# Optimization experiments

Measured on AMD Instinct MI355X. Metric: run time of the kernel, lower is better.

The kernel has to match this reference:

```python
import jax, jax.numpy as jnp
import numpy as np

N = 4096
IN_F = 512
OUT_F = 64
N_HEADS = 8
ALPHA = 0.2
NEG_INF = -9e15


def setup_inputs() -> dict:
    key = jax.random.key(0)
    k1, k2, k3, k4 = jax.random.split(key, 4)
    h = jax.random.normal(k1, (N, IN_F), dtype=jnp.float32)
    adj = jax.random.randint(k2, (N, N), 0, 2, dtype=jnp.int32)
    W = jax.random.normal(k3, (IN_F, OUT_F * N_HEADS), dtype=jnp.float32) * (1.414 / np.sqrt(IN_F))
    a = jax.random.normal(k4, (2 * OUT_F, 1), dtype=jnp.float32) * 0.1
    return {"h": h, "adj": adj, "W": W, "a": a}


def reference(h, adj, W, a):
    # Wh: [N, H, F]
    Wh = (h @ W).reshape(N, N_HEADS, OUT_F)
    # The all-pairs concat + matmul with a ([2F,1], shared across heads)
    # decomposes exactly: e[i,j,h] = leakyrelu(Wh[i,h]@a[:F] + Wh[j,h]@a[F:])
    a_src = a[:OUT_F, 0]
    a_dst = a[OUT_F:, 0]
    src = jnp.einsum('nhf,f->nh', Wh, a_src)  # [N, H]
    dst = jnp.einsum('nhf,f->nh', Wh, a_dst)  # [N, H]
    e = src[:, None, :] + dst[None, :, :]      # [N, N, H]
    e = jnp.where(e > 0, e, ALPHA * e)         # leaky relu
    e = jnp.where(adj[:, :, None] > 0, e, NEG_INF)
    attention = jax.nn.softmax(e, axis=1)      # softmax over neighbors j
    h_prime = jnp.einsum('ijh,jhf->ihf', attention, Wh)  # [N, H, F]
    out = h_prime.reshape(N, N_HEADS * OUT_F)
    return jax.nn.elu(out)
```

## Files before the change

kernel.cpp:

```cpp
#include <hip/hip_runtime.h>
#include <hip/hip_bf16.h>


typedef unsigned short ushort_t;
typedef __attribute__((ext_vector_type(8))) short bf16x8;
typedef __attribute__((ext_vector_type(4))) float f32x4;

#define LOG2E 1.4426950408889634f

__device__ __forceinline__ ushort_t f2bf(float x) {
    unsigned u = __builtin_bit_cast(unsigned, x);
    u += 0x7FFFu + ((u >> 16) & 1u);
    return (ushort_t)(u >> 16);
}

__global__ __launch_bounds__(256) void transpose_w(const float* __restrict__ W,
                                                   ushort_t* __restrict__ WT) {
    __shared__ ushort_t t[32][33];
    int bx = blockIdx.x & 15, by = blockIdx.x >> 4;
    int tx = threadIdx.x & 31, ty = threadIdx.x >> 5;
#pragma unroll
    for (int i = 0; i < 32; i += 8)
        t[ty + i][tx] = f2bf(W[(by * 32 + ty + i) * 512 + bx * 32 + tx]);
    __syncthreads();
#pragma unroll
    for (int i = 0; i < 32; i += 8)
        WT[(bx * 32 + ty + i) * 512 + by * 32 + tx] = t[tx][ty + i];
}

__global__ __launch_bounds__(256, 4) void gemm_whT(const ushort_t* __restrict__ WT,
                                                   const float* __restrict__ h,
                                                   const float* __restrict__ a,
                                                   ushort_t* __restrict__ WhT,
                                                   float* __restrict__ expA,
                                                   float* __restrict__ expC,
                                                   float* __restrict__ expB,
                                                   float* __restrict__ expD) {
    __shared__ __align__(16) ushort_t Al[2][64][72];
    __shared__ __align__(16) ushort_t Bl[2][64][72];
    __shared__ float asrc[64], adst[64];
    __shared__ float sred[2][4][64];
    int tid = threadIdx.x;
    int wave = tid >> 6, lane = tid & 63, quad = lane >> 4, nn = lane & 15;
    int mb = blockIdx.x & 7, nb = blockIdx.x >> 3;
    if (tid < 64) {
        asrc[tid] = a[tid] * LOG2E;
        adst[tid] = a[64 + tid] * LOG2E;
    }
    int r = tid >> 2, s0 = tid & 3;
    const ushort_t* Ag = WT + (unsigned)((mb * 64 + r) * 512 + s0 * 8);
    const float* Bg = h + (unsigned)((nb * 64 + r) * 512 + s0 * 8);
    bf16x8 pA0 = *(const bf16x8*)(Ag);
    bf16x8 pA1 = *(const bf16x8*)(Ag + 32);
    float4 pb0 = *(const float4*)(Bg);
    float4 pb1 = *(const float4*)(Bg + 4);
    float4 pb2 = *(const float4*)(Bg + 32);
    float4 pb3 = *(const float4*)(Bg + 36);
    f32x4 acc[4] = {};
#pragma unroll 2
    for (int t = 0; t < 8; t++) {
        int cb = t & 1;
        *(bf16x8*)&Al[cb][r][s0 * 8] = pA0;
        *(bf16x8*)&Al[cb][r][s0 * 8 + 32] = pA1;
        bf16x8 bv;
        bv[0] = (short)f2bf(pb0.x); bv[1] = (short)f2bf(pb0.y);
        bv[2] = (short)f2bf(pb0.z); bv[3] = (short)f2bf(pb0.w);
        bv[4] = (short)f2bf(pb1.x); bv[5] = (short)f2bf(pb1.y);
        bv[6] = (short)f2bf(pb1.z); bv[7] = (short)f2bf(pb1.w);
        *(bf16x8*)&Bl[cb][r][s0 * 8] = bv;
        bv[0] = (short)f2bf(pb2.x); bv[1] = (short)f2bf(pb2.y);
        bv[2] = (short)f2bf(pb2.z); bv[3] = (short)f2bf(pb2.w);
        bv[4] = (short)f2bf(pb3.x); bv[5] = (short)f2bf(pb3.y);
        bv[6] = (short)f2bf(pb3.z); bv[7] = (short)f2bf(pb3.w);
        *(bf16x8*)&Bl[cb][r][s0 * 8 + 32] = bv;
        if (t < 7) {
            int ko = (t + 1) * 64;
            pA0 = *(const bf16x8*)(Ag + ko);
            pA1 = *(const bf16x8*)(Ag + ko + 32);
            pb0 = *(const float4*)(Bg + ko);
            pb1 = *(const float4*)(Bg + ko + 4);
            pb2 = *(const float4*)(Bg + ko + 32);
            pb3 = *(const float4*)(Bg + ko + 36);
        }
        if (t > 0) {
            int pb = cb ^ 1;
            bf16x8 af0 = *(const bf16x8*)&Al[pb][wave * 16 + nn][quad * 8];
            bf16x8 af1 = *(const bf16x8*)&Al[pb][wave * 16 + nn][32 + quad * 8];
#pragma unroll
            for (int nt = 0; nt < 4; nt++) {
                bf16x8 b0 = *(const bf16x8*)&Bl[pb][nt * 16 + nn][quad * 8];
                bf16x8 b1 = *(const bf16x8*)&Bl[pb][nt * 16 + nn][32 + quad * 8];
                acc[nt] = __builtin_amdgcn_mfma_f32_16x16x32_bf16(af0, b0, acc[nt], 0, 0, 0);
                acc[nt] = __builtin_amdgcn_mfma_f32_16x16x32_bf16(af1, b1, acc[nt], 0, 0, 0);
            }
        }
        __syncthreads();
    }
    {
        bf16x8 af0 = *(const bf16x8*)&Al[1][wave * 16 + nn][quad * 8];
        bf16x8 af1 = *(const bf16x8*)&Al[1][wave * 16 + nn][32 + quad * 8];
#pragma unroll
        for (int nt = 0; nt < 4; nt++) {
            bf16x8 b0 = *(const bf16x8*)&Bl[1][nt * 16 + nn][quad * 8];
            bf16x8 b1 = *(const bf16x8*)&Bl[1][nt * 16 + nn][32 + quad * 8];
            acc[nt] = __builtin_amdgcn_mfma_f32_16x16x32_bf16(af0, b0, acc[nt], 0, 0, 0);
            acc[nt] = __builtin_amdgcn_mfma_f32_16x16x32_bf16(af1, b1, acc[nt], 0, 0, 0);
        }
    }
    int row0 = mb * 64 + wave * 16 + quad * 4;
    int col0 = nb * 64 + nn;
    int f0i = wave * 16 + quad * 4;
#pragma unroll
    for (int nt = 0; nt < 4; nt++) {
        float s = 0.f, d = 0.f;
#pragma unroll
        for (int rr = 0; rr < 4; rr++) {
            float v = acc[nt][rr];
            WhT[(unsigned)((row0 + rr) * 4096 + col0 + nt * 16)] = f2bf(v);
            s += v * asrc[f0i + rr];
            d += v * adst[f0i + rr];
        }
        s += __shfl_xor(s, 16); s += __shfl_xor(s, 32);
        d += __shfl_xor(d, 16); d += __shfl_xor(d, 32);
        if (quad == 0) { sred[0][wave][nt * 16 + nn] = s; sred[1][wave][nt * 16 + nn] = d; }
    }
    __syncthreads();
    if (tid < 64) {
        float s = sred[0][0][tid] + sred[0][1][tid] + sred[0][2][tid] + sred[0][3][tid];
        unsigned idx = mb * 4096 + nb * 64 + tid;
        expA[idx] = __builtin_amdgcn_exp2f(s);
        expC[idx] = __builtin_amdgcn_exp2f(0.2f * s);
    } else if (tid < 128) {
        int c = tid - 64;
        float d = sred[1][0][c] + sred[1][1][c] + sred[1][2][c] + sred[1][3][c];
        unsigned idx = mb * 4096 + nb * 64 + c;
        expB[idx] = __builtin_amdgcn_exp2f(d);
        expD[idx] = __builtin_amdgcn_exp2f(0.2f * d);
    }
}

__global__ __launch_bounds__(512, 4) void gat_attn(const int* __restrict__ adj,
                                                   const ushort_t* __restrict__ WhT,
                                                   const float* __restrict__ expA,
                                                   const float* __restrict__ expC,
                                                   const float* __restrict__ expB,
                                                   const float* __restrict__ expD,
                                                   float* __restrict__ out) {
    __shared__ __align__(16) ushort_t Vb[2][128][72];
    __shared__ __align__(16) ushort_t Pb[2][2][32][72];
    __shared__ float denoml[2][32];
    int tid = threadIdx.x;
    int wave = tid >> 6, lane = tid & 63, quad = lane >> 4, nn = lane & 15;
    int hb = blockIdx.x >> 7, ib = blockIdx.x & 127;
    int i0 = ib * 32;
    int hh = tid >> 8, tt = tid & 255;
    int pi = tt >> 3, jo = tt & 7;
    int head = hb * 2 + hh;
    float Ai = expA[head * 4096 + i0 + pi];
    float Ci = expC[head * 4096 + i0 + pi];
    const int* adjP = adj + (unsigned)(i0 + pi) * 4096 + jo * 8;
    const float* Bp = expB + (unsigned)head * 4096 + jo * 8;
    const float* Dp = expD + (unsigned)head * 4096 + jo * 8;
    int vr = tid >> 3, vcs = tid & 7;
    const ushort_t* Vg0 = WhT + (unsigned)(hb * 128 + vr) * 4096 + vcs * 8;
    const ushort_t* Vg1 = Vg0 + 64u * 4096u;
    int jhalf = wave >> 2, ws = wave & 3;
    int strip = ws & 1, whead = ws >> 1;
    f32x4 acc[4] = {};
    float dpart = 0.f;
    int4 pa[2][2]; bf16x8 pvv[2][2]; float4 pBD[2][4];
    pa[0][0] = *(const int4*)(adjP);
    pa[0][1] = *(const int4*)(adjP + 4);
    pvv[0][0] = *(const bf16x8*)(Vg0);
    pvv[0][1] = *(const bf16x8*)(Vg1);
    pBD[0][0] = *(const float4*)(Bp);
    pBD[0][1] = *(const float4*)(Bp + 4);
    pBD[0][2] = *(const float4*)(Dp);
    pBD[0][3] = *(const float4*)(Dp + 4);
#pragma unroll 2
    for (int k = 0; k < 64; k++) {
        int cb = k & 1;
        float4 Bv0 = pBD[cb][0], Bv1 = pBD[cb][1];
        float4 Dv0 = pBD[cb][2], Dv1 = pBD[cb][3];
        int4 a0 = pa[cb][0], a1 = pa[cb][1];
        unsigned w0, w1, w2, w3, w4, w5, w6, w7;
        {
            float w;
            w = fmaxf(Ai * Bv0.x, Ci * Dv0.x);
            w0 = __builtin_bit_cast(unsigned, w) & 0xFFFF0000u;  w0 = a0.x > 0 ? w0 : 0u;
            w = fmaxf(Ai * Bv0.y, Ci * Dv0.y);
            w1 = __builtin_bit_cast(unsigned, w) & 0xFFFF0000u;  w1 = a0.y > 0 ? w1 : 0u;
            w = fmaxf(Ai * Bv0.z, Ci * Dv0.z);
            w2 = __builtin_bit_cast(unsigned, w) & 0xFFFF0000u;  w2 = a0.z > 0 ? w2 : 0u;
            w = fmaxf(Ai * Bv0.w, Ci * Dv0.w);
            w3 = __builtin_bit_cast(unsigned, w) & 0xFFFF0000u;  w3 = a0.w > 0 ? w3 : 0u;
            w = fmaxf(Ai * Bv1.x, Ci * Dv1.x);
            w4 = __builtin_bit_cast(unsigned, w) & 0xFFFF0000u;  w4 = a1.x > 0 ? w4 : 0u;
            w = fmaxf(Ai * Bv1.y, Ci * Dv1.y);
            w5 = __builtin_bit_cast(unsigned, w) & 0xFFFF0000u;  w5 = a1.y > 0 ? w5 : 0u;
            w = fmaxf(Ai * Bv1.z, Ci * Dv1.z);
            w6 = __builtin_bit_cast(unsigned, w) & 0xFFFF0000u;  w6 = a1.z > 0 ? w6 : 0u;
            w = fmaxf(Ai * Bv1.w, Ci * Dv1.w);
            w7 = __builtin_bit_cast(unsigned, w) & 0xFFFF0000u;  w7 = a1.w > 0 ? w7 : 0u;
        }
        dpart += __builtin_bit_cast(float, w0) + __builtin_bit_cast(float, w1)
               + __builtin_bit_cast(float, w2) + __builtin_bit_cast(float, w3)
               + __builtin_bit_cast(float, w4) + __builtin_bit_cast(float, w5)
               + __builtin_bit_cast(float, w6) + __builtin_bit_cast(float, w7);
        uint4 pq;
        pq.x = __builtin_amdgcn_perm(w1, w0, 0x07060302u);
        pq.y = __builtin_amdgcn_perm(w3, w2, 0x07060302u);
        pq.z = __builtin_amdgcn_perm(w5, w4, 0x07060302u);
        pq.w = __builtin_amdgcn_perm(w7, w6, 0x07060302u);
        *(uint4*)&Pb[cb][hh][pi][jo * 8] = pq;
        *(bf16x8*)&Vb[cb][vr][vcs * 8] = pvv[cb][0];
        *(bf16x8*)&Vb[cb][64 + vr][vcs * 8] = pvv[cb][1];
        if (k < 63) {
            const int* ap = adjP + (k + 1) * 64;
            pa[cb ^ 1][0] = *(const int4*)(ap);
            pa[cb ^ 1][1] = *(const int4*)(ap + 4);
            pBD[cb ^ 1][0] = *(const float4*)(Bp + (k + 1) * 64);
            pBD[cb ^ 1][1] = *(const float4*)(Bp + (k + 1) * 64 + 4);
            pBD[cb ^ 1][2] = *(const float4*)(Dp + (k + 1) * 64);
            pBD[cb ^ 1][3] = *(const float4*)(Dp + (k + 1) * 64 + 4);
            pvv[cb ^ 1][0] = *(const bf16x8*)(Vg0 + (k + 1) * 64);
            pvv[cb ^ 1][1] = *(const bf16x8*)(Vg1 + (k + 1) * 64);
        }
        if (k > 0) {
            int pbuf = cb ^ 1;
            bf16x8 af = *(const bf16x8*)&Pb[pbuf][whead][strip * 16 + nn][jhalf * 32 + quad * 8];
#pragma unroll
            for (int nt = 0; nt < 4; nt++) {
                bf16x8 bv = *(const bf16x8*)&Vb[pbuf][whead * 64 + nt * 16 + nn][jhalf * 32 + quad * 8];
                acc[nt] = __builtin_amdgcn_mfma_f32_16x16x32_bf16(af, bv, acc[nt], 0, 0, 0);
            }
        }
        __syncthreads();
    }
    {
        bf16x8 af = *(const bf16x8*)&Pb[1][whead][strip * 16 + nn][jhalf * 32 + quad * 8];
#pragma unroll
        for (int nt = 0; nt < 4; nt++) {
            bf16x8 bv = *(const bf16x8*)&Vb[1][whead * 64 + nt * 16 + nn][jhalf * 32 + quad * 8];
            acc[nt] = __builtin_amdgcn_mfma_f32_16x16x32_bf16(af, bv, acc[nt], 0, 0, 0);
        }
    }
    float dsum = dpart;
    dsum += __shfl_xor(dsum, 1);
    dsum += __shfl_xor(dsum, 2);
    dsum += __shfl_xor(dsum, 4);
    if ((tid & 7) == 0) denoml[hh][pi] = dsum;
    __syncthreads();
    float (*cmb)[64][8] = reinterpret_cast<float (*)[64][8]>(&Vb[0][0][0]);
    if (jhalf == 1) {
        *(f32x4*)&cmb[ws][lane][0] = acc[0];
        *(f32x4*)&cmb[ws][lane][4] = acc[1];
    }
    __syncthreads();
    if (jhalf == 0) {
        f32x4 o0 = acc[0] + *(const f32x4*)&cmb[ws][lane][0];
        f32x4 o1 = acc[1] + *(const f32x4*)&cmb[ws][lane][4];
#pragma unroll
        for (int rr = 0; rr < 4; rr++) {
            int il = strip * 16 + quad * 4 + rr;
            float dnm = fmaxf(denoml[whead][il], 1e-30f);
            float v0 = o0[rr] / dnm;
            float v1 = o1[rr] / dnm;
            v0 = v0 > 0.f ? v0 : __expf(v0) - 1.f;
            v1 = v1 > 0.f ? v1 : __expf(v1) - 1.f;
            unsigned oi = (unsigned)(i0 + il) * 512 + hb * 128 + whead * 64 + nn;
            out[oi] = v0;
            out[oi + 16] = v1;
        }
    }
    __syncthreads();
    if (jhalf == 1) {
        *(f32x4*)&cmb[ws][lane][0] = acc[2];
        *(f32x4*)&cmb[ws][lane][4] = acc[3];
    }
    __syncthreads();
    if (jhalf == 0) {
        f32x4 o0 = acc[2] + *(const f32x4*)&cmb[ws][lane][0];
        f32x4 o1 = acc[3] + *(const f32x4*)&cmb[ws][lane][4];
#pragma unroll
        for (int rr = 0; rr < 4; rr++) {
            int il = strip * 16 + quad * 4 + rr;
            float dnm = fmaxf(denoml[whead][il], 1e-30f);
            float v0 = o0[rr] / dnm;
            float v1 = o1[rr] / dnm;
            v0 = v0 > 0.f ? v0 : __expf(v0) - 1.f;
            v1 = v1 > 0.f ? v1 : __expf(v1) - 1.f;
            unsigned oi = (unsigned)(i0 + il) * 512 + hb * 128 + whead * 64 + 32 + nn;
            out[oi] = v0;
            out[oi + 16] = v1;
        }
    }
}

extern "C" void kernel_launch(void* const* d_in, const int* in_sizes, int n_in,
                              void* d_out, int out_size, void* d_ws, size_t ws_size,
                              hipStream_t stream) {
    const float* h   = (const float*)d_in[0];
    const int*   adj = (const int*)d_in[1];
    const float* W   = (const float*)d_in[2];
    const float* a   = (const float*)d_in[3];

    char* ws = (char*)d_ws;
    ushort_t* WhT = (ushort_t*)ws;
    ushort_t* WT  = (ushort_t*)(ws + (4u << 20));
    float* expA = (float*)(ws + (4u << 20) + (512u << 10));
    float* expC = expA + 8 * 4096;
    float* expB = expC + 8 * 4096;
    float* expD = expB + 8 * 4096;

    transpose_w<<<256, 256, 0, stream>>>(W, WT);
    gemm_whT<<<512, 256, 0, stream>>>(WT, h, a, WhT, expA, expC, expB, expD);
    gat_attn<<<512, 512, 0, stream>>>(adj, WhT, expA, expC, expB, expD,
                                      (float*)d_out);
}
```

Baseline: 191.4 us.

## Bit-pack adjacency, load V straight to registers, compute denominator with MFMA

Adds a pre-pass that packs the int32 adjacency matrix into a bitmask, which gat_attn decodes with bitfield extracts. In the original, each of the 4 head-pair blocks per row tile reread the full int32 adjacency. gat_attn also drops the LDS staging of V and loads Wh fragments directly from global memory into registers. It computes the softmax denominator with an extra MFMA against a ones vector instead of scalar adds and shuffles. The costs are an extra kernel launch, a full pass over adj in the pack kernel, and less coalesced V loads, since each wave now fetches its own fragments.

```diff
diff --git a/kernel.cpp b/kernel.cpp
--- a/kernel.cpp
+++ b/kernel.cpp
@@ -12,6 +12,34 @@
     unsigned u = __builtin_bit_cast(unsigned, x);
     u += 0x7FFFu + ((u >> 16) & 1u);
     return (ushort_t)(u >> 16);
+}
+
+__global__ __launch_bounds__(256) void pack_adj(const int* __restrict__ adj,
+                                                unsigned char* __restrict__ pk) {
+    int wv = threadIdx.x >> 6, lane = threadIdx.x & 63;
+    int row = blockIdx.x * 4 + wv;
+    const int* ap = adj + (unsigned)row * 4096 + lane;
+    unsigned char* pp = pk + (unsigned)row * 512;
+    int jo = lane & 7;
+#pragma unroll 2
+    for (int k4 = 0; k4 < 16; k4++) {
+        int v0 = ap[(k4 * 4 + 0) * 64];
+        int v1 = ap[(k4 * 4 + 1) * 64];
+        int v2 = ap[(k4 * 4 + 2) * 64];
+        int v3 = ap[(k4 * 4 + 3) * 64];
+        unsigned long long m0 = __ballot(v0 > 0);
+        unsigned long long m1 = __ballot(v1 > 0);
+        unsigned long long m2 = __ballot(v2 > 0);
+        unsigned long long m3 = __ballot(v3 > 0);
+        if (lane < 8) {
+            int sh = jo * 8;
+            unsigned b = ((unsigned)(m0 >> sh) & 0xFFu)
+                       | (((unsigned)(m1 >> sh) & 0xFFu) << 8)
+                       | (((unsigned)(m2 >> sh) & 0xFFu) << 16)
+                       | (((unsigned)(m3 >> sh) & 0xFFu) << 24);
+            *(unsigned*)(pp + jo * 64 + k4 * 4) = b;
+        }
+    }
 }
 
 __global__ __launch_bounds__(256) void transpose_w(const float* __restrict__ W,
@@ -139,16 +167,15 @@
     }
 }
 
-__global__ __launch_bounds__(512, 4) void gat_attn(const int* __restrict__ adj,
+__global__ __launch_bounds__(512, 4) void gat_attn(const unsigned char* __restrict__ pk,
                                                    const ushort_t* __restrict__ WhT,
                                                    const float* __restrict__ expA,
                                                    const float* __restrict__ expC,
                                                    const float* __restrict__ expB,
                                                    const float* __restrict__ expD,
                                                    float* __restrict__ out) {
-    __shared__ __align__(16) ushort_t Vb[2][128][72];
     __shared__ __align__(16) ushort_t Pb[2][2][32][72];
-    __shared__ float denoml[2][32];
+    __shared__ float denomp[2][2][32];
     int tid = threadIdx.x;
     int wave = tid >> 6, lane = tid & 63, quad = lane >> 4, nn = lane & 15;
     int hb = blockIdx.x >> 7, ib = blockIdx.x & 127;
@@ -158,100 +185,106 @@
     int head = hb * 2 + hh;
     float Ai = expA[head * 4096 + i0 + pi];
     float Ci = expC[head * 4096 + i0 + pi];
-    const int* adjP = adj + (unsigned)(i0 + pi) * 4096 + jo * 8;
+    const unsigned char* mp = pk + (unsigned)(i0 + pi) * 512 + jo * 64;
     const float* Bp = expB + (unsigned)head * 4096 + jo * 8;
     const float* Dp = expD + (unsigned)head * 4096 + jo * 8;
-    int vr = tid >> 3, vcs = tid & 7;
-    const ushort_t* Vg0 = WhT + (unsigned)(hb * 128 + vr) * 4096 + vcs * 8;
-    const ushort_t* Vg1 = Vg0 + 64u * 4096u;
     int jhalf = wave >> 2, ws = wave & 3;
     int strip = ws & 1, whead = ws >> 1;
+    const ushort_t* Vbase = WhT + (unsigned)(hb * 128 + whead * 64 + nn) * 4096
+                          + jhalf * 32 + quad * 8;
+    bf16x8 onef;
+#pragma unroll
+    for (int i = 0; i < 8; i++) onef[i] = (short)0x3F80;
     f32x4 acc[4] = {};
-    float dpart = 0.f;
-    int4 pa[2][2]; bf16x8 pvv[2][2]; float4 pBD[2][4];
-    pa[0][0] = *(const int4*)(adjP);
-    pa[0][1] = *(const int4*)(adjP + 4);
-    pvv[0][0] = *(const bf16x8*)(Vg0);
-    pvv[0][1] = *(const bf16x8*)(Vg1);
+    f32x4 accd = {};
+    float4 pBD[2][4]; bf16x8 pV[2][4];
     pBD[0][0] = *(const float4*)(Bp);
     pBD[0][1] = *(const float4*)(Bp + 4);
     pBD[0][2] = *(const float4*)(Dp);
     pBD[0][3] = *(const float4*)(Dp + 4);
-#pragma unroll 2
-    for (int k = 0; k < 64; k++) {
-        int cb = k & 1;
-        float4 Bv0 = pBD[cb][0], Bv1 = pBD[cb][1];
-        float4 Dv0 = pBD[cb][2], Dv1 = pBD[cb][3];
-        int4 a0 = pa[cb][0], a1 = pa[cb][1];
-        unsigned w0, w1, w2, w3, w4, w5, w6, w7;
-        {
-            float w;
-            w = fmaxf(Ai * Bv0.x, Ci * Dv0.x);
-            w0 = __builtin_bit_cast(unsigned, w) & 0xFFFF0000u;  w0 = a0.x > 0 ? w0 : 0u;
-            w = fmaxf(Ai * Bv0.y, Ci * Dv0.y);
-            w1 = __builtin_bit_cast(unsigned, w) & 0xFFFF0000u;  w1 = a0.y > 0 ? w1 : 0u;
-            w = fmaxf(Ai * Bv0.z, Ci * Dv0.z);
-            w2 = __builtin_bit_cast(unsigned, w) & 0xFFFF0000u;  w2 = a0.z > 0 ? w2 : 0u;
-            w = fmaxf(Ai * Bv0.w, Ci * Dv0.w);
-            w3 = __builtin_bit_cast(unsigned, w) & 0xFFFF0000u;  w3 = a0.w > 0 ? w3 : 0u;
-            w = fmaxf(Ai * Bv1.x, Ci * Dv1.x);
-            w4 = __builtin_bit_cast(unsigned, w) & 0xFFFF0000u;  w4 = a1.x > 0 ? w4 : 0u;
-            w = fmaxf(Ai * Bv1.y, Ci * Dv1.y);
-            w5 = __builtin_bit_cast(unsigned, w) & 0xFFFF0000u;  w5 = a1.y > 0 ? w5 : 0u;
-            w = fmaxf(Ai * Bv1.z, Ci * Dv1.z);
-            w6 = __builtin_bit_cast(unsigned, w) & 0xFFFF0000u;  w6 = a1.z > 0 ? w6 : 0u;
-            w = fmaxf(Ai * Bv1.w, Ci * Dv1.w);
-            w7 = __builtin_bit_cast(unsigned, w) & 0xFFFF0000u;  w7 = a1.w > 0 ? w7 : 0u;
-        }
-        dpart += __builtin_bit_cast(float, w0) + __builtin_bit_cast(float, w1)
-               + __builtin_bit_cast(float, w2) + __builtin_bit_cast(float, w3)
-               + __builtin_bit_cast(float, w4) + __builtin_bit_cast(float, w5)
-               + __builtin_bit_cast(float, w6) + __builtin_bit_cast(float, w7);
-        uint4 pq;
-        pq.x = __builtin_amdgcn_perm(w1, w0, 0x07060302u);
-        pq.y = __builtin_amdgcn_perm(w3, w2, 0x07060302u);
-        pq.z = __builtin_amdgcn_perm(w5, w4, 0x07060302u);
-        pq.w = __builtin_amdgcn_perm(w7, w6, 0x07060302u);
-        *(uint4*)&Pb[cb][hh][pi][jo * 8] = pq;
-        *(bf16x8*)&Vb[cb][vr][vcs * 8] = pvv[cb][0];
-        *(bf16x8*)&Vb[cb][64 + vr][vcs * 8] = pvv[cb][1];
-        if (k < 63) {
-            const int* ap = adjP + (k + 1) * 64;
-            pa[cb ^ 1][0] = *(const int4*)(ap);
-            pa[cb ^ 1][1] = *(const int4*)(ap + 4);
-            pBD[cb ^ 1][0] = *(const float4*)(Bp + (k + 1) * 64);
-            pBD[cb ^ 1][1] = *(const float4*)(Bp + (k + 1) * 64 + 4);
-            pBD[cb ^ 1][2] = *(const float4*)(Dp + (k + 1) * 64);
-            pBD[cb ^ 1][3] = *(const float4*)(Dp + (k + 1) * 64 + 4);
-            pvv[cb ^ 1][0] = *(const bf16x8*)(Vg0 + (k + 1) * 64);
-            pvv[cb ^ 1][1] = *(const bf16x8*)(Vg1 + (k + 1) * 64);
-        }
-        if (k > 0) {
+#pragma unroll
+    for (int nt = 0; nt < 4; nt++)
+        pV[0][nt] = *(const bf16x8*)(Vbase + nt * 65536);
+    unsigned mcur = *(const unsigned*)(mp);
+    for (int t = 0; t < 16; t++) {
+        unsigned mnext = (t < 15) ? *(const unsigned*)(mp + (t + 1) * 4) : 0u;
+#pragma unroll
+        for (int u = 0; u < 4; u++) {
+            int k = t * 4 + u;
+            int cb = u & 1;
             int pbuf = cb ^ 1;
-            bf16x8 af = *(const bf16x8*)&Pb[pbuf][whead][strip * 16 + nn][jhalf * 32 + quad * 8];
-#pragma unroll
-            for (int nt = 0; nt < 4; nt++) {
-                bf16x8 bv = *(const bf16x8*)&Vb[pbuf][whead * 64 + nt * 16 + nn][jhalf * 32 + quad * 8];
-                acc[nt] = __builtin_amdgcn_mfma_f32_16x16x32_bf16(af, bv, acc[nt], 0, 0, 0);
-            }
-        }
-        __syncthreads();
+            float4 Bv0 = pBD[cb][0], Bv1 = pBD[cb][1];
+            float4 Dv0 = pBD[cb][2], Dv1 = pBD[cb][3];
+            unsigned w0, w1, w2, w3, w4, w5, w6, w7;
+            {
+                float w;
+                w = fmaxf(Ai * Bv0.x, Ci * Dv0.x);
+                w0 = __builtin_bit_cast(unsigned, w) & 0xFFFF0000u;
+                w0 &= (unsigned)__builtin_amdgcn_sbfe(mcur, u * 8 + 0, 1);
+                w = fmaxf(Ai * Bv0.y, Ci * Dv0.y);
+                w1 = __builtin_bit_cast(unsigned, w) & 0xFFFF0000u;
+                w1 &= (unsigned)__builtin_amdgcn_sbfe(mcur, u * 8 + 1, 1);
+                w = fmaxf(Ai * Bv0.z, Ci * Dv0.z);
+                w2 = __builtin_bit_cast(unsigned, w) & 0xFFFF0000u;
+                w2 &= (unsigned)__builtin_amdgcn_sbfe(mcur, u * 8 + 2, 1);
+                w = fmaxf(Ai * Bv0.w, Ci * Dv0.w);
+                w3 = __builtin_bit_cast(unsigned, w) & 0xFFFF0000u;
+                w3 &= (unsigned)__builtin_amdgcn_sbfe(mcur, u * 8 + 3, 1);
+                w = fmaxf(Ai * Bv1.x, Ci * Dv1.x);
+                w4 = __builtin_bit_cast(unsigned, w) & 0xFFFF0000u;
+                w4 &= (unsigned)__builtin_amdgcn_sbfe(mcur, u * 8 + 4, 1);
+                w = fmaxf(Ai * Bv1.y, Ci * Dv1.y);
+                w5 = __builtin_bit_cast(unsigned, w) & 0xFFFF0000u;
+                w5 &= (unsigned)__builtin_amdgcn_sbfe(mcur, u * 8 + 5, 1);
+                w = fmaxf(Ai * Bv1.z, Ci * Dv1.z);
+                w6 = __builtin_bit_cast(unsigned, w) & 0xFFFF0000u;
+                w6 &= (unsigned)__builtin_amdgcn_sbfe(mcur, u * 8 + 6, 1);
+                w = fmaxf(Ai * Bv1.w, Ci * Dv1.w);
+                w7 = __builtin_bit_cast(unsigned, w) & 0xFFFF0000u;
+                w7 &= (unsigned)__builtin_amdgcn_sbfe(mcur, u * 8 + 7, 1);
+            }
+            uint4 pq;
+            pq.x = __builtin_amdgcn_perm(w1, w0, 0x07060302u);
+            pq.y = __builtin_amdgcn_perm(w3, w2, 0x07060302u);
+            pq.z = __builtin_amdgcn_perm(w5, w4, 0x07060302u);
+            pq.w = __builtin_amdgcn_perm(w7, w6, 0x07060302u);
+            *(uint4*)&Pb[cb][hh][pi][jo * 8] = pq;
+            if (k < 63) {
+                pBD[pbuf][0] = *(const float4*)(Bp + (k + 1) * 64);
+                pBD[pbuf][1] = *(const float4*)(Bp + (k + 1) * 64 + 4);
+                pBD[pbuf][2] = *(const float4*)(Dp + (k + 1) * 64);
+                pBD[pbuf][3] = *(const float4*)(Dp + (k + 1) * 64 + 4);
+            }
+            if (k > 0) {
+                bf16x8 af = *(const bf16x8*)&Pb[pbuf][whead][strip * 16 + nn][jhalf * 32 + quad * 8];
+#pragma unroll
+                for (int nt = 0; nt < 4; nt++)
+                    acc[nt] = __builtin_amdgcn_mfma_f32_16x16x32_bf16(af, pV[pbuf][nt], acc[nt], 0, 0, 0);
+                accd = __builtin_amdgcn_mfma_f32_16x16x32_bf16(af, onef, accd, 0, 0, 0);
+            }
+            if (k < 63) {
+#pragma unroll
+                for (int nt = 0; nt < 4; nt++)
+                    pV[pbuf][nt] = *(const bf16x8*)(Vbase + nt * 65536 + (k + 1) * 64);
+            }
+            __syncthreads();
+        }
+        mcur = mnext;
     }
     {
         bf16x8 af = *(const bf16x8*)&Pb[1][whead][strip * 16 + nn][jhalf * 32 + quad * 8];
 #pragma unroll
-        for (int nt = 0; nt < 4; nt++) {
-            bf16x8 bv = *(const bf16x8*)&Vb[1][whead * 64 + nt * 16 + nn][jhalf * 32 + quad * 8];
-            acc[nt] = __builtin_amdgcn_mfma_f32_16x16x32_bf16(af, bv, acc[nt], 0, 0, 0);
-        }
-    }
-    float dsum = dpart;
-    dsum += __shfl_xor(dsum, 1);
-    dsum += __shfl_xor(dsum, 2);
-    dsum += __shfl_xor(dsum, 4);
-    if ((tid & 7) == 0) denoml[hh][pi] = dsum;
-    __syncthreads();
-    float (*cmb)[64][8] = reinterpret_cast<float (*)[64][8]>(&Vb[0][0][0]);
+        for (int nt = 0; nt < 4; nt++)
+            acc[nt] = __builtin_amdgcn_mfma_f32_16x16x32_bf16(af, pV[1][nt], acc[nt], 0, 0, 0);
+        accd = __builtin_amdgcn_mfma_f32_16x16x32_bf16(af, onef, accd, 0, 0, 0);
+    }
+    if ((lane & 15) == 0) {
+#pragma unroll
+        for (int rr = 0; rr < 4; rr++)
+            denomp[jhalf][whead][strip * 16 + quad * 4 + rr] = accd[rr];
+    }
+    __syncthreads();
+    float (*cmb)[64][8] = reinterpret_cast<float (*)[64][8]>(&Pb[0][0][0][0]);
     if (jhalf == 1) {
         *(f32x4*)&cmb[ws][lane][0] = acc[0];
         *(f32x4*)&cmb[ws][lane][4] = acc[1];
@@ -263,7 +296,7 @@
 #pragma unroll
         for (int rr = 0; rr < 4; rr++) {
             int il = strip * 16 + quad * 4 + rr;
-            float dnm = fmaxf(denoml[whead][il], 1e-30f);
+            float dnm = fmaxf(denomp[0][whead][il] + denomp[1][whead][il], 1e-30f);
             float v0 = o0[rr] / dnm;
             float v1 = o1[rr] / dnm;
             v0 = v0 > 0.f ? v0 : __expf(v0) - 1.f;
@@ -285,7 +318,7 @@
 #pragma unroll
         for (int rr = 0; rr < 4; rr++) {
             int il = strip * 16 + quad * 4 + rr;
-            float dnm = fmaxf(denoml[whead][il], 1e-30f);
+            float dnm = fmaxf(denomp[0][whead][il] + denomp[1][whead][il], 1e-30f);
             float v0 = o0[rr] / dnm;
             float v1 = o1[rr] / dnm;
             v0 = v0 > 0.f ? v0 : __expf(v0) - 1.f;
@@ -312,9 +345,11 @@
     float* expC = expA + 8 * 4096;
     float* expB = expC + 8 * 4096;
     float* expD = expB + 8 * 4096;
-
+    unsigned char* pkm = (unsigned char*)(ws + (5u << 20));
+
+    pack_adj<<<1024, 256, 0, stream>>>(adj, pkm);
     transpose_w<<<256, 256, 0, stream>>>(W, WT);
     gemm_whT<<<512, 256, 0, stream>>>(WT, h, a, WhT, expA, expC, expB, expD);
-    gat_attn<<<512, 512, 0, stream>>>(adj, WhT, expA, expC, expB, expD,
+    gat_attn<<<512, 512, 0, stream>>>(pkm, WhT, expA, expC, expB, expD,
                                       (float*)d_out);
 }
```

Result: slower. 268.1 us (+40.1%).
